# Optimization experiments

Measured on AMD Instinct MI355X. Metric: run time of the kernel, lower is better.

## Reference

```python
import jax, jax.numpy as jnp
import numpy as np
from jax import lax

C, NH, HC, HID, P = 192, 8, 64, 512, 16
B, H, W = 2, 128, 128
EPS = 1e-5


def setup_inputs() -> dict:
    key = jax.random.key(0)
    ks = jax.random.split(key, 12)
    f = lambda i, shape: jax.random.normal(ks[i], shape, jnp.float32) * 0.05
    return dict(
        x=jax.random.normal(ks[0], (B, C, H, W), jnp.float32),
        ln1_g=jnp.ones((C,), jnp.float32), ln1_b=jnp.zeros((C,), jnp.float32),
        wq=f(1, (HID, C)), wk=f(2, (HID, C)), wv=f(3, (HID, C)),
        wo=f(4, (C, HID)), bo=jnp.zeros((C,), jnp.float32),
        dw_w=f(5, (C, 1, 3, 3)), dw_b=jnp.zeros((C,), jnp.float32),
        mlp_w=f(6, (C, 2 * C)), mlp_b=jnp.zeros((C,), jnp.float32),
        ln2_g=jnp.ones((C,), jnp.float32), ln2_b=jnp.zeros((C,), jnp.float32),
        c1_w=f(7, (C, C)), c1_b=jnp.zeros((C,), jnp.float32),
        res_w=f(8, (C, 1, 3, 3)), res_b=jnp.zeros((C,), jnp.float32),
        c2_w=f(9, (C, C)), c2_b=jnp.zeros((C,), jnp.float32),
    )


def ln_ch(x, g, b):
    # LayerNorm over the channel dim of an NCHW tensor (biased variance, like torch)
    m = x.mean(1, keepdims=True)
    v = ((x - m) ** 2).mean(1, keepdims=True)
    return (x - m) / jnp.sqrt(v + EPS) * g[None, :, None, None] + b[None, :, None, None]


def inorm(x):
    # InstanceNorm2d, affine=False
    m = x.mean((2, 3), keepdims=True)
    v = ((x - m) ** 2).mean((2, 3), keepdims=True)
    return (x - m) / jnp.sqrt(v + EPS)


def conv1x1(x, w, b=None):
    y = jnp.einsum('oc,bchw->bohw', w, x)
    return y if b is None else y + b[None, :, None, None]


def dwconv(x, w, b):
    y = lax.conv_general_dilated(x, w, (1, 1), 'SAME',
                                 feature_group_count=x.shape[1],
                                 dimension_numbers=('NCHW', 'OIHW', 'NCHW'))
    return y + b[None, :, None, None]


def res_block(x, w, b):
    return jax.nn.gelu(inorm(dwconv(x, w, b)), approximate=False) + x


def dpsa(x, ln_g, ln_b, wq, wk, wv, wo, bo):
    Bs, _, Hs, Ws = x.shape
    xn = ln_ch(x, ln_g, ln_b)

    def proj(w):  # -> (B*NH, H, W, HC)
        t = jnp.einsum('oc,bchw->bohw', w, xn)
        return t.reshape(Bs * NH, HC, Hs, Ws).transpose(0, 2, 3, 1)

    l2n = lambda t: t / jnp.maximum(jnp.linalg.norm(t, axis=-1, keepdims=True), 1e-12)
    q = l2n(proj(wq))
    k = l2n(proj(wk))
    v = proj(wv)

    qs = q.sum((1, 2))                                   # (BH, HC)
    h_scores = jnp.einsum('bc,bhc->bh', qs, k.sum(2))    # (BH, H)
    w_scores = jnp.einsum('bc,bwc->bw', qs, k.sum(1))    # (BH, W)
    _, h_idx = lax.top_k(h_scores, P)
    _, w_idx = lax.top_k(w_scores, P)

    k = jnp.take_along_axis(k, h_idx[:, :, None, None], axis=1)   # (BH, P, W, HC)
    v = jnp.take_along_axis(v, h_idx[:, :, None, None], axis=1)
    k = jnp.take_along_axis(k, w_idx[:, None, :, None], axis=2)   # (BH, P, P, HC)
    v = jnp.take_along_axis(v, w_idx[:, None, :, None], axis=2)

    qf = q.reshape(Bs * NH, Hs * Ws, HC)
    kf = k.reshape(Bs * NH, P * P, HC)
    vf = v.reshape(Bs * NH, P * P, HC)
    attn = jax.nn.softmax(jnp.einsum('bqc,bkc->bqk', qf, kf), axis=-1)
    out = jnp.einsum('bqk,bkc->bqc', attn, vf)
    out = out.reshape(Bs, NH, Hs, Ws, HC).transpose(0, 1, 4, 2, 3).reshape(Bs, NH * HC, Hs, Ws)
    return conv1x1(out, wo, bo)


def reference(x, ln1_g, ln1_b, wq, wk, wv, wo, bo, dw_w, dw_b, mlp_w, mlp_b,
              ln2_g, ln2_b, c1_w, c1_b, res_w, res_b, c2_w, c2_b):
    global_branch = dpsa(x, ln1_g, ln1_b, wq, wk, wv, wo, bo)
    local_branch = dwconv(x, dw_w, dw_b)
    f = jnp.concatenate((local_branch, global_branch), axis=1)
    f = conv1x1(f, mlp_w, mlp_b) + x
    y = ln_ch(f, ln2_g, ln2_b)
    y = jax.nn.gelu(inorm(conv1x1(y, c1_w, c1_b)), approximate=False)
    y = res_block(y, res_w, res_b)
    y = inorm(conv1x1(y, c2_w, c2_b))
    return y
```

## Files before the change

kernel.cpp:

```cpp
#include <hip/hip_runtime.h>
#include <math.h>

constexpr int kC   = 192;
constexpr int kNH  = 8;
constexpr int kHC  = 64;
constexpr int kHID = 512;
constexpr int kP   = 16;
constexpr int kB   = 2;
constexpr int kH   = 128;
constexpr int kW   = 128;
constexpr int kHW  = kH * kW;
constexpr int kN   = kB * kHW;
constexpr float kEPS = 1e-5f;

typedef __attribute__((ext_vector_type(8))) short bf16x8;
typedef __attribute__((ext_vector_type(4))) float f32x4;

__device__ inline unsigned short f2bf(float f) {
    unsigned int u = __builtin_bit_cast(unsigned int, f);
    unsigned int r = (u + 0x7FFFu + ((u >> 16) & 1u)) >> 16;
    return (unsigned short)r;
}
__device__ inline float bf2f(unsigned short u) {
    return __builtin_bit_cast(float, (unsigned int)u << 16);
}
__device__ inline unsigned int cvtpk(float lo, float hi) {
    unsigned int r;
    asm("v_cvt_pk_bf16_f32 %0, %1, %2" : "=v"(r) : "v"(lo), "v"(hi));
    return r;
}
__device__ inline unsigned long long pk4(float a, float b, float c, float d) {
    return (unsigned long long)cvtpk(a, b) | ((unsigned long long)cvtpk(c, d) << 32);
}
__device__ inline f32x4 ubf4(unsigned long long u) {
    f32x4 r;
    r[0] = bf2f((unsigned short)u);
    r[1] = bf2f((unsigned short)(u >> 16));
    r[2] = bf2f((unsigned short)(u >> 32));
    r[3] = bf2f((unsigned short)(u >> 48));
    return r;
}
__device__ inline float gelu_f(float x) {
    return 0.5f * x * (1.0f + erff(x * 0.70710678118654752f));
}

__global__ void prep_kernel(float* __restrict__ zbase,
                            const float* wq, const float* wk, const float* wm,
                            const float* c1, const float* c2,
                            const float* wo, const float* mlp_b, const float* bo,
                            unsigned short* wqb, unsigned short* wkb,
                            unsigned short* mlpb1, unsigned short* c1b, unsigned short* c2b,
                            unsigned short* w2pb, float* bp2)
{
    int i = blockIdx.x * 256 + threadIdx.x;
    if (i < 2304) { zbase[i] = 0.f; return; }
    i -= 2304;
    if (i < 98304) { wqb[i] = f2bf(wq[i]); return; }
    i -= 98304;
    if (i < 98304) { wkb[i] = f2bf(wk[i]); return; }
    i -= 98304;
    if (i < 36864) { int o = i / 192, k = i - o * 192; mlpb1[i] = f2bf(wm[o * 384 + k]); return; }
    i -= 36864;
    if (i < 36864) { c1b[i] = f2bf(c1[i]); return; }
    i -= 36864;
    if (i < 36864) { c2b[i] = f2bf(c2[i]); return; }
    i -= 36864;
    if (i < 98304) {
        int o = i >> 9, j = i & 511;
        const float* a = wm + o * 384 + 192;
        float s = 0.f;
        for (int c = 0; c < 192; ++c) s += a[c] * wo[c * 512 + j];
        w2pb[o * 512 + j] = f2bf(s);
        if (j == 0) {
            float t = mlp_b[o];
            for (int c = 0; c < 192; ++c) t += a[c] * bo[c];
            bp2[o] = t;
        }
    }
}

__global__ __launch_bounds__(256) void txln_kernel(const float* __restrict__ x,
                                                   unsigned short* __restrict__ xpb,
                                                   unsigned short* __restrict__ xnb,
                                                   const float* __restrict__ g,
                                                   const float* __restrict__ bb)
{
    __shared__ float tile[192][65];
    __shared__ float red[2][4][64];
    __shared__ float pms[64], prs[64];
    int hw0 = blockIdx.x * 64;
    int b   = blockIdx.y;
    int tid = threadIdx.x;
    for (int i = tid; i < 192 * 64; i += 256) {
        int c = i >> 6, p = i & 63;
        tile[c][p] = x[(size_t)(b * kC + c) * kHW + hw0 + p];
    }
    __syncthreads();
    {
        int p = tid & 63, qt = tid >> 6;
        float s = 0.f, ss = 0.f;
        for (int c = qt * 48; c < qt * 48 + 48; ++c) {
            float v = tile[c][p]; s += v; ss += v * v;
        }
        red[0][qt][p] = s; red[1][qt][p] = ss;
    }
    __syncthreads();
    if (tid < 64) {
        float s  = red[0][0][tid] + red[0][1][tid] + red[0][2][tid] + red[0][3][tid];
        float ss = red[1][0][tid] + red[1][1][tid] + red[1][2][tid] + red[1][3][tid];
        float m = s * (1.0f / kC);
        float var = ss * (1.0f / kC) - m * m;
        pms[tid] = m;
        prs[tid] = rsqrtf(var + kEPS);
    }
    __syncthreads();
    for (int i = tid; i < 64 * 192; i += 256) {
        int p = i / 192, c = i - p * 192;
        float raw = tile[c][p];
        size_t oi = (size_t)(b * kHW + hw0 + p) * kC + c;
        xpb[oi] = f2bf(raw);
        xnb[oi] = f2bf((raw - pms[p]) * prs[p] * g[c] + bb[c]);
    }
}

__global__ void ln_pm_bf16_kernel(const unsigned short* __restrict__ in,
                                  unsigned short* __restrict__ out,
                                  const float* __restrict__ g, const float* __restrict__ bb)
{
    int t = blockIdx.x * 256 + threadIdx.x;
    int n = t >> 2, q = t & 3;
    const unsigned long long* ip = (const unsigned long long*)(in + (size_t)n * kC) + q * 12;
    f32x4 v[12];
    float s = 0.f, ss = 0.f;
#pragma unroll
    for (int r = 0; r < 12; ++r) {
        v[r] = ubf4(ip[r]);
        s  += (v[r][0] + v[r][1]) + (v[r][2] + v[r][3]);
        ss += (v[r][0]*v[r][0] + v[r][1]*v[r][1]) + (v[r][2]*v[r][2] + v[r][3]*v[r][3]);
    }
    s  += __shfl_xor(s, 1);  s  += __shfl_xor(s, 2);
    ss += __shfl_xor(ss, 1); ss += __shfl_xor(ss, 2);
    float m  = s * (1.0f / kC);
    float var = ss * (1.0f / kC) - m * m;
    float rs = rsqrtf(var + kEPS);
    unsigned long long* op = (unsigned long long*)(out + (size_t)n * kC) + q * 12;
#pragma unroll
    for (int r = 0; r < 12; ++r) {
        f32x4 gg = *(const f32x4*)(g + q * 48 + r * 4);
        f32x4 bv = *(const f32x4*)(bb + q * 48 + r * 4);
        op[r] = pk4((v[r][0]-m)*rs*gg[0] + bv[0], (v[r][1]-m)*rs*gg[1] + bv[1],
                    (v[r][2]-m)*rs*gg[2] + bv[2], (v[r][3]-m)*rs*gg[3] + bv[3]);
    }
}

#define MGEMM_CORE(KVAL, APTR, BPTR)                                              \
    {                                                                             \
        const unsigned short* Ap = APTR;                                          \
        const unsigned short* Bp = BPTR;                                          \
        _Pragma("unroll 2")                                                       \
        for (int k = 0; k < KVAL; k += 32) {                                      \
            bf16x8 a0 = *(const bf16x8*)(Ap + k);                                 \
            bf16x8 a1 = *(const bf16x8*)(Ap + (size_t)16 * KVAL + k);             \
            bf16x8 b0 = *(const bf16x8*)(Bp + k);                                 \
            bf16x8 b1 = *(const bf16x8*)(Bp + (size_t)16 * KVAL + k);             \
            bf16x8 b2 = *(const bf16x8*)(Bp + (size_t)32 * KVAL + k);             \
            bf16x8 b3 = *(const bf16x8*)(Bp + (size_t)48 * KVAL + k);             \
            acc[0][0] = __builtin_amdgcn_mfma_f32_16x16x32_bf16(a0, b0, acc[0][0], 0, 0, 0); \
            acc[0][1] = __builtin_amdgcn_mfma_f32_16x16x32_bf16(a0, b1, acc[0][1], 0, 0, 0); \
            acc[0][2] = __builtin_amdgcn_mfma_f32_16x16x32_bf16(a0, b2, acc[0][2], 0, 0, 0); \
            acc[0][3] = __builtin_amdgcn_mfma_f32_16x16x32_bf16(a0, b3, acc[0][3], 0, 0, 0); \
            acc[1][0] = __builtin_amdgcn_mfma_f32_16x16x32_bf16(a1, b0, acc[1][0], 0, 0, 0); \
            acc[1][1] = __builtin_amdgcn_mfma_f32_16x16x32_bf16(a1, b1, acc[1][1], 0, 0, 0); \
            acc[1][2] = __builtin_amdgcn_mfma_f32_16x16x32_bf16(a1, b2, acc[1][2], 0, 0, 0); \
            acc[1][3] = __builtin_amdgcn_mfma_f32_16x16x32_bf16(a1, b3, acc[1][3], 0, 0, 0); \
        }                                                                         \
    }

__device__ void mgemm_l2_body(int nblk, int head,
                              const unsigned short* __restrict__ A,
                              const unsigned short* __restrict__ B,
                              unsigned short* __restrict__ out,
                              float* __restrict__ red_out)
{
    __shared__ float ssq[2][2][4][16];
    __shared__ float rbuf[2][2][4][2][4];
    int nB = nblk * 128, oB = head * 64;
    int w = threadIdx.x >> 6, lane = threadIdx.x & 63;
    int l15 = lane & 15, g = lane >> 4;
    int wm = w & 1, wn = w >> 1;

    f32x4 acc[2][4];
#pragma unroll
    for (int mt = 0; mt < 2; ++mt)
#pragma unroll
        for (int nt = 0; nt < 4; ++nt) acc[mt][nt] = (f32x4){0.f,0.f,0.f,0.f};

    MGEMM_CORE(192, A + (size_t)(oB + wm * 32 + l15) * 192 + 8 * g,
                    B + (size_t)(nB + wn * 64 + l15) * 192 + 8 * g);

#pragma unroll
    for (int nt = 0; nt < 4; ++nt) {
        float s = 0.f;
#pragma unroll
        for (int mt = 0; mt < 2; ++mt) {
            f32x4 a = acc[mt][nt];
            s += (a[0]*a[0] + a[1]*a[1]) + (a[2]*a[2] + a[3]*a[3]);
        }
        s += __shfl_xor(s, 16);
        s += __shfl_xor(s, 32);
        if (g == 0) ssq[wm][wn][nt][l15] = s;
    }
    __syncthreads();

    float sc[4];
#pragma unroll
    for (int nt = 0; nt < 4; ++nt) {
        float ss2 = ssq[0][wn][nt][l15] + ssq[1][wn][nt][l15];
        sc[nt] = 1.0f / fmaxf(sqrtf(ss2), 1e-12f);
    }

#pragma unroll
    for (int nt = 0; nt < 4; ++nt) {
        int n = nB + wn * 64 + nt * 16 + l15;
#pragma unroll
        for (int mt = 0; mt < 2; ++mt) {
            int o = oB + wm * 32 + mt * 16 + 4 * g;
            f32x4 v = acc[mt][nt];
            *(unsigned long long*)(out + (size_t)n * kHID + o) =
                pk4(v[0]*sc[nt], v[1]*sc[nt], v[2]*sc[nt], v[3]*sc[nt]);
        }
    }

    float sred[2][4] = {};
#pragma unroll
    for (int nt = 0; nt < 4; ++nt)
#pragma unroll
        for (int mt = 0; mt < 2; ++mt) {
            f32x4 a = acc[mt][nt];
            sred[mt][0] += a[0] * sc[nt];
            sred[mt][1] += a[1] * sc[nt];
            sred[mt][2] += a[2] * sc[nt];
            sred[mt][3] += a[3] * sc[nt];
        }
#pragma unroll
    for (int off = 1; off < 16; off <<= 1)
#pragma unroll
        for (int mt = 0; mt < 2; ++mt)
#pragma unroll
            for (int r = 0; r < 4; ++r)
                sred[mt][r] += __shfl_xor(sred[mt][r], off);
    if (l15 == 0)
#pragma unroll
        for (int mt = 0; mt < 2; ++mt)
#pragma unroll
            for (int r = 0; r < 4; ++r)
                rbuf[wm][wn][g][mt][r] = sred[mt][r];
    __syncthreads();
    if (threadIdx.x < 64) {
        int o = threadIdx.x;
        int wm2 = o >> 5, mt2 = (o >> 4) & 1, g2 = (o >> 2) & 3, r2 = o & 3;
        float v = rbuf[wm2][0][g2][mt2][r2] + rbuf[wm2][1][g2][mt2][r2];
        int row = (nB & (kHW - 1)) >> 7;
        int b = nB >> 14;
        int bh = b * 8 + head;
        red_out[((size_t)(bh * 128 + row)) * 64 + o] = v;
    }
}

__device__ void dwconv_body(int idx, const unsigned short* __restrict__ in,
                            unsigned short* __restrict__ out,
                            const float* __restrict__ wt, const float* __restrict__ bias)
{
    int n = idx / 48;
    int c0 = (idx - n * 48) * 4;
    int hw = n & (kHW - 1);
    int h = hw >> 7, ww = hw & 127;
    f32x4 s = *(const f32x4*)(bias + c0);
#pragma unroll
    for (int dy = -1; dy <= 1; ++dy) {
        int hh = h + dy;
        if (hh < 0 || hh >= kH) continue;
#pragma unroll
        for (int dx = -1; dx <= 1; ++dx) {
            int wx = ww + dx;
            if (wx < 0 || wx >= kW) continue;
            f32x4 v = ubf4(*(const unsigned long long*)(in + (size_t)(n + dy * kW + dx) * kC + c0));
            int t = (dy + 1) * 3 + (dx + 1);
            s[0] += v[0] * wt[(c0 + 0) * 9 + t];
            s[1] += v[1] * wt[(c0 + 1) * 9 + t];
            s[2] += v[2] * wt[(c0 + 2) * 9 + t];
            s[3] += v[3] * wt[(c0 + 3) * 9 + t];
        }
    }
    *(unsigned long long*)(out + (size_t)n * kC + c0) = pk4(s[0], s[1], s[2], s[3]);
}

__global__ __launch_bounds__(256) void branch_kernel(
    const unsigned short* __restrict__ wqb, const unsigned short* __restrict__ wkb,
    const unsigned short* __restrict__ xnb, const unsigned short* __restrict__ xpb,
    unsigned short* __restrict__ qpb, unsigned short* __restrict__ kpb,
    float* __restrict__ qpart, float* __restrict__ ksum_h,
    unsigned short* __restrict__ lb,
    const float* __restrict__ dw_w, const float* __restrict__ dw_b)
{
    int id = blockIdx.x;
    if (id < 2048) {
        mgemm_l2_body(id & 255, id >> 8, wqb, xnb, qpb, qpart);
    } else if (id < 4096) {
        id -= 2048;
        mgemm_l2_body(id & 255, id >> 8, wkb, xnb, kpb, ksum_h);
    } else {
        dwconv_body((id - 4096) * 256 + threadIdx.x, xpb, lb, dw_w, dw_b);
    }
}

__global__ void sum_h_kernel(const unsigned short* __restrict__ buf, float* __restrict__ out)
{
    __shared__ float red[4][64];
    int w = blockIdx.x, bh = blockIdx.y;
    int hc = threadIdx.x & 63, seg = threadIdx.x >> 6;
    int b = bh >> 3, nh = bh & 7;
    const unsigned short* p = buf + (size_t)(b * kHW + seg * 32 * kW + w) * kHID + nh * kHC + hc;
    float s = 0.f;
    for (int h = 0; h < 32; ++h) s += bf2f(p[(size_t)h * kW * kHID]);
    red[seg][hc] = s;
    __syncthreads();
    if (threadIdx.x < 64)
        out[((size_t)bh * kW + w) * kHC + threadIdx.x] =
            red[0][threadIdx.x] + red[1][threadIdx.x] + red[2][threadIdx.x] + red[3][threadIdx.x];
}

__global__ __launch_bounds__(256) void mgemm_is_kernel(
    const unsigned short* __restrict__ A, const unsigned short* __restrict__ B,
    unsigned short* __restrict__ out, const float* __restrict__ bias,
    float* __restrict__ accp)
{
    __shared__ float sa[2][64], qa[2][64];
    int nB = blockIdx.x * 128, oB = blockIdx.y * 64;
    int w = threadIdx.x >> 6, lane = threadIdx.x & 63;
    int l15 = lane & 15, g = lane >> 4;
    int wm = w & 1, wn = w >> 1;

    f32x4 acc[2][4];
#pragma unroll
    for (int mt = 0; mt < 2; ++mt)
#pragma unroll
        for (int nt = 0; nt < 4; ++nt) acc[mt][nt] = (f32x4){0.f,0.f,0.f,0.f};

    MGEMM_CORE(192, A + (size_t)(oB + wm * 32 + l15) * 192 + 8 * g,
                    B + (size_t)(nB + wn * 64 + l15) * 192 + 8 * g);

    f32x4 vv[2][4];
#pragma unroll
    for (int mt = 0; mt < 2; ++mt)
#pragma unroll
        for (int nt = 0; nt < 4; ++nt) {
            int o = oB + wm * 32 + mt * 16 + 4 * g;
            int n = nB + wn * 64 + nt * 16 + l15;
            f32x4 v = acc[mt][nt] + *(const f32x4*)(bias + o);
            vv[mt][nt] = v;
            *(unsigned long long*)(out + (size_t)n * kC + o) = pk4(v[0], v[1], v[2], v[3]);
        }
    float s2[2][4] = {}, q2[2][4] = {};
#pragma unroll
    for (int mt = 0; mt < 2; ++mt)
#pragma unroll
        for (int nt = 0; nt < 4; ++nt)
#pragma unroll
            for (int r = 0; r < 4; ++r) {
                float v = vv[mt][nt][r];
                s2[mt][r] += v; q2[mt][r] += v * v;
            }
#pragma unroll
    for (int off = 1; off < 16; off <<= 1)
#pragma unroll
        for (int mt = 0; mt < 2; ++mt)
#pragma unroll
            for (int r = 0; r < 4; ++r) {
                s2[mt][r] += __shfl_xor(s2[mt][r], off);
                q2[mt][r] += __shfl_xor(q2[mt][r], off);
            }
    if (l15 == 0)
#pragma unroll
        for (int mt = 0; mt < 2; ++mt)
#pragma unroll
            for (int r = 0; r < 4; ++r) {
                int ol = wm * 32 + mt * 16 + 4 * g + r;
                sa[wn][ol] = s2[mt][r];
                qa[wn][ol] = q2[mt][r];
            }
    __syncthreads();
    if (threadIdx.x < 128) {
        int ol = threadIdx.x & 63, st = threadIdx.x >> 6;
        float v = st ? (qa[0][ol] + qa[1][ol]) : (sa[0][ol] + sa[1][ol]);
        int b = nB >> 14;
        atomicAdd(&accp[(size_t)(b * kC + oB + ol) * 2 + st], v);
    }
}

__global__ __launch_bounds__(256) void mgemm_mlp_kernel(
    const unsigned short* __restrict__ A1, const unsigned short* __restrict__ B1,
    const unsigned short* __restrict__ A2, const unsigned short* __restrict__ B2,
    unsigned short* __restrict__ out, const float* __restrict__ bp2,
    const unsigned short* __restrict__ res)
{
    int nB = blockIdx.x * 128, oB = blockIdx.y * 64;
    int w = threadIdx.x >> 6, lane = threadIdx.x & 63;
    int l15 = lane & 15, g = lane >> 4;
    int wm = w & 1, wn = w >> 1;

    f32x4 acc[2][4];
#pragma unroll
    for (int mt = 0; mt < 2; ++mt)
#pragma unroll
        for (int nt = 0; nt < 4; ++nt) acc[mt][nt] = (f32x4){0.f,0.f,0.f,0.f};

    MGEMM_CORE(192, A1 + (size_t)(oB + wm * 32 + l15) * 192 + 8 * g,
                    B1 + (size_t)(nB + wn * 64 + l15) * 192 + 8 * g);
    MGEMM_CORE(512, A2 + (size_t)(oB + wm * 32 + l15) * 512 + 8 * g,
                    B2 + (size_t)(nB + wn * 64 + l15) * 512 + 8 * g);

#pragma unroll
    for (int mt = 0; mt < 2; ++mt)
#pragma unroll
        for (int nt = 0; nt < 4; ++nt) {
            int o = oB + wm * 32 + mt * 16 + 4 * g;
            int n = nB + wn * 64 + nt * 16 + l15;
            f32x4 v = acc[mt][nt];
            v[0] += bp2[o]; v[1] += bp2[o+1]; v[2] += bp2[o+2]; v[3] += bp2[o+3];
            v += ubf4(*(const unsigned long long*)(res + (size_t)n * kC + o));
            *(unsigned long long*)(out + (size_t)n * kC + o) = pk4(v[0], v[1], v[2], v[3]);
        }
}

__global__ void score_topk_kernel(const float* __restrict__ qpart,
                                  const float* __restrict__ ksum_h,
                                  const float* __restrict__ ksum_w,
                                  int* __restrict__ hidx, int* __restrict__ widx)
{
    __shared__ float qsl[2][64];
    __shared__ float hs[128], ws[128];
    int bh = blockIdx.x;
    int tid = threadIdx.x;
    int hc = tid & 63, grp = tid >> 6;
    {
        const float* qp = qpart + ((size_t)bh * 128 + grp * 64) * 64 + hc;
        float s = 0.f;
        for (int i = 0; i < 64; ++i) s += qp[(size_t)i * 64];
        qsl[grp][hc] = s;
    }
    __syncthreads();
    if (tid < 64) qsl[0][tid] += qsl[1][tid];
    __syncthreads();
    {
        const float* kh = ksum_h + ((size_t)bh * 128 + tid) * 64;
        const float* kw = ksum_w + ((size_t)bh * 128 + tid) * 64;
        float sh = 0.f, sw = 0.f;
        for (int c = 0; c < 64; ++c) {
            float q = qsl[0][c];
            sh += q * kh[c];
            sw += q * kw[c];
        }
        hs[tid] = sh; ws[tid] = sw;
    }
    __syncthreads();
    int sel = tid >> 6;
    const float* sc = sel ? ws : hs;
    int* out = (sel ? widx : hidx) + bh * kP;
    int lane = tid & 63;
    float v0 = sc[lane], v1 = sc[lane + 64];
    int i0 = lane, i1 = lane + 64;
    for (int p = 0; p < kP; ++p) {
        float bv; int bi;
        if (v1 > v0) { bv = v1; bi = i1; } else { bv = v0; bi = i0; }
#pragma unroll
        for (int off = 1; off < 64; off <<= 1) {
            float ov = __shfl_xor(bv, off);
            int   oi = __shfl_xor(bi, off);
            if (ov > bv || (ov == bv && oi < bi)) { bv = ov; bi = oi; }
        }
        if (lane == 0) out[p] = bi;
        if (i0 == bi) v0 = -INFINITY;
        if (i1 == bi) v1 = -INFINITY;
    }
}

__global__ void gather_kv_kernel(const unsigned short* __restrict__ kpb,
                                 const unsigned short* __restrict__ xnb,
                                 const float* __restrict__ wv,
                                 const int* __restrict__ hidx, const int* __restrict__ widx,
                                 unsigned short* __restrict__ kf, unsigned short* __restrict__ vfT)
{
    int bh = blockIdx.y, p1 = blockIdx.x;
    int b = bh >> 3, nh = bh & 7;
    int hc = threadIdx.x & 63, pg = threadIdx.x >> 6;
    int hrow = hidx[bh * kP + p1];
    int o = nh * kHC + hc;
    const float* wvp = wv + (size_t)o * kC;
    for (int p2 = pg; p2 < kP; p2 += 4) {
        int wcol = widx[bh * kP + p2];
        int n = b * kHW + hrow * kW + wcol;
        int kidx = p1 * kP + p2;
        kf[((size_t)bh * 256 + kidx) * 64 + hc] = kpb[(size_t)n * kHID + nh * kHC + hc];
        const unsigned int* xr = (const unsigned int*)(xnb + (size_t)n * kC);
        float s = 0.f;
        for (int c2 = 0; c2 < kC / 2; ++c2) {
            unsigned int u = xr[c2];
            s += wvp[c2 * 2]     * bf2f((unsigned short)(u & 0xffff));
            s += wvp[c2 * 2 + 1] * bf2f((unsigned short)(u >> 16));
        }
        vfT[((size_t)bh * 64 + hc) * 256 + kidx] = f2bf(s);
    }
}

__global__ __launch_bounds__(256) void attn_kernel(
    const unsigned short* __restrict__ qpb, unsigned short* __restrict__ ob,
    const unsigned short* __restrict__ kf, const unsigned short* __restrict__ vfT)
{
    __shared__ unsigned short pls[64 * 256];
    __shared__ float lred[4][4][16];

    int bh = blockIdx.y; int b = bh >> 3, nh = bh & 7;
    int nbase = b * kHW + blockIdx.x * 128;
    int tid = threadIdx.x;
    int w = tid >> 6, lane = tid & 63, l15 = lane & 15, g = lane >> 4;

    const unsigned short* kfb = kf + (size_t)bh * 256 * 64;
    bf16x8 ak[4][2];
#pragma unroll
    for (int mt = 0; mt < 4; ++mt)
#pragma unroll
        for (int kt = 0; kt < 2; ++kt)
            ak[mt][kt] = *(const bf16x8*)&kfb[(size_t)(w * 64 + mt * 16 + l15) * 64 + kt * 32 + 8 * g];

    const unsigned short* vfb = vfT + (size_t)bh * 64 * 256;

#pragma unroll
    for (int sub = 0; sub < 2; ++sub) {
        int n0 = nbase + sub * 64;
        bf16x8 bq[4][2];
#pragma unroll
        for (int nt = 0; nt < 4; ++nt)
#pragma unroll
            for (int kt = 0; kt < 2; ++kt)
                bq[nt][kt] = *(const bf16x8*)(qpb + (size_t)(n0 + nt * 16 + l15) * kHID
                                              + nh * kHC + kt * 32 + 8 * g);

        f32x4 acc[4][4];
#pragma unroll
        for (int mt = 0; mt < 4; ++mt)
#pragma unroll
            for (int nt = 0; nt < 4; ++nt) acc[mt][nt] = (f32x4){0.f,0.f,0.f,0.f};

#pragma unroll
        for (int kt = 0; kt < 2; ++kt)
#pragma unroll
            for (int mt = 0; mt < 4; ++mt)
#pragma unroll
                for (int nt = 0; nt < 4; ++nt)
                    acc[mt][nt] = __builtin_amdgcn_mfma_f32_16x16x32_bf16(
                        ak[mt][kt], bq[nt][kt], acc[mt][nt], 0, 0, 0);

        if (sub) __syncthreads();

        float lpart[4] = {0.f, 0.f, 0.f, 0.f};
#pragma unroll
        for (int mt = 0; mt < 4; ++mt)
#pragma unroll
            for (int nt = 0; nt < 4; ++nt) {
                float e0 = __expf(acc[mt][nt][0]);
                float e1 = __expf(acc[mt][nt][1]);
                float e2 = __expf(acc[mt][nt][2]);
                float e3 = __expf(acc[mt][nt][3]);
                lpart[nt] += (e0 + e1) + (e2 + e3);
                int qq = nt * 16 + l15;
                int k0 = w * 64 + mt * 16 + 4 * g;
                int kx = k0 ^ ((qq & 7) << 3);
                *(unsigned long long*)&pls[qq * 256 + kx] = pk4(e0, e1, e2, e3);
            }
#pragma unroll
        for (int nt = 0; nt < 4; ++nt) {
            lpart[nt] += __shfl_xor(lpart[nt], 16);
            lpart[nt] += __shfl_xor(lpart[nt], 32);
        }
        if (g == 0)
#pragma unroll
            for (int nt = 0; nt < 4; ++nt) lred[w][nt][l15] = lpart[nt];
        __syncthreads();

        f32x4 oacc[4];
#pragma unroll
        for (int nt = 0; nt < 4; ++nt) oacc[nt] = (f32x4){0.f,0.f,0.f,0.f};

#pragma unroll
        for (int ks = 0; ks < 8; ++ks) {
            bf16x8 av = *(const bf16x8*)&vfb[(size_t)(w * 16 + l15) * 256 + ks * 32 + 8 * g];
#pragma unroll
            for (int nt = 0; nt < 4; ++nt) {
                int qq = nt * 16 + l15;
                int kx = (ks * 32 + 8 * g) ^ ((qq & 7) << 3);
                bf16x8 bp = *(const bf16x8*)&pls[qq * 256 + kx];
                oacc[nt] = __builtin_amdgcn_mfma_f32_16x16x32_bf16(av, bp, oacc[nt], 0, 0, 0);
            }
        }

#pragma unroll
        for (int nt = 0; nt < 4; ++nt) {
            float l = lred[0][nt][l15] + lred[1][nt][l15] + lred[2][nt][l15] + lred[3][nt][l15];
            float inv = 1.0f / l;
            int qq = nt * 16 + l15;
            int hc0 = w * 16 + 4 * g;
            *(unsigned long long*)(ob + (size_t)(n0 + qq) * kHID + nh * kHC + hc0) =
                pk4(oacc[nt][0] * inv, oacc[nt][1] * inv, oacc[nt][2] * inv, oacc[nt][3] * inv);
        }
    }
}

__global__ void istats_bf16_kernel(const unsigned short* __restrict__ in, float* __restrict__ acc)
{
    int n0 = blockIdx.x * 64;
    int b = n0 >> 14;
    int c = threadIdx.x;
    float s = 0.f, ss = 0.f;
    for (int p = 0; p < 64; ++p) {
        float v = bf2f(in[(size_t)(n0 + p) * kC + c]);
        s += v; ss += v * v;
    }
    atomicAdd(&acc[(size_t)(b * kC + c) * 2],     s);
    atomicAdd(&acc[(size_t)(b * kC + c) * 2 + 1], ss);
}

__device__ inline void inorm_ms(const float* acc, int b, int c, float& m, float& rs)
{
    float s  = acc[(size_t)(b * kC + c) * 2];
    float ss = acc[(size_t)(b * kC + c) * 2 + 1];
    m = s * (1.0f / kHW);
    float var = ss * (1.0f / kHW) - m * m;
    rs = rsqrtf(var + kEPS);
}

__global__ void dwconv_gelu_kernel(const unsigned short* __restrict__ t1,
                                   const float* __restrict__ acc0,
                                   unsigned short* __restrict__ rout,
                                   const float* __restrict__ wt, const float* __restrict__ bias)
{
    int idx = blockIdx.x * 256 + threadIdx.x;
    int n = idx / 48;
    int c0 = (idx - n * 48) * 4;
    int hw = n & (kHW - 1);
    int b = n >> 14;
    int h = hw >> 7, ww = hw & 127;
    float m[4], rs[4];
#pragma unroll
    for (int j = 0; j < 4; ++j) inorm_ms(acc0, b, c0 + j, m[j], rs[j]);
    f32x4 s = *(const f32x4*)(bias + c0);
#pragma unroll
    for (int dy = -1; dy <= 1; ++dy) {
        int hh = h + dy;
        if (hh < 0 || hh >= kH) continue;
#pragma unroll
        for (int dx = -1; dx <= 1; ++dx) {
            int wx = ww + dx;
            if (wx < 0 || wx >= kW) continue;
            f32x4 v = ubf4(*(const unsigned long long*)(t1 + (size_t)(n + dy * kW + dx) * kC + c0));
            int t = (dy + 1) * 3 + (dx + 1);
#pragma unroll
            for (int j = 0; j < 4; ++j)
                s[j] += gelu_f((v[j] - m[j]) * rs[j]) * wt[(c0 + j) * 9 + t];
        }
    }
    *(unsigned long long*)(rout + (size_t)n * kC + c0) = pk4(s[0], s[1], s[2], s[3]);
}

__global__ void apply_res_kernel(const unsigned short* __restrict__ r,
                                 const unsigned short* __restrict__ t1,
                                 const float* __restrict__ acc1, const float* __restrict__ acc0,
                                 unsigned short* __restrict__ out)
{
    int idx = blockIdx.x * 256 + threadIdx.x;
    int n = idx / 48;
    int c0 = (idx - n * 48) * 4;
    int b = n >> 14;
    f32x4 vr = ubf4(*(const unsigned long long*)(r  + (size_t)n * kC + c0));
    f32x4 vt = ubf4(*(const unsigned long long*)(t1 + (size_t)n * kC + c0));
    f32x4 o;
#pragma unroll
    for (int j = 0; j < 4; ++j) {
        float m1, rs1, m0, rs0;
        inorm_ms(acc1, b, c0 + j, m1, rs1);
        inorm_ms(acc0, b, c0 + j, m0, rs0);
        o[j] = gelu_f((vr[j] - m1) * rs1) + gelu_f((vt[j] - m0) * rs0);
    }
    *(unsigned long long*)(out + (size_t)n * kC + c0) = pk4(o[0], o[1], o[2], o[3]);
}

__global__ __launch_bounds__(256) void final_kernel(const unsigned short* __restrict__ in,
                                                    const float* __restrict__ acc,
                                                    float* __restrict__ out)
{
    __shared__ unsigned short tile[192][68];
    int n0 = blockIdx.x * 64;
    int b = n0 >> 14;
    int hw0 = n0 & (kHW - 1);
    int tid = threadIdx.x;
    for (int i = tid; i < 64 * 48; i += 256) {
        int p = i / 48, cq = i - p * 48;
        unsigned long long u = *(const unsigned long long*)(in + (size_t)(n0 + p) * kC + cq * 4);
        tile[cq * 4 + 0][p] = (unsigned short)u;
        tile[cq * 4 + 1][p] = (unsigned short)(u >> 16);
        tile[cq * 4 + 2][p] = (unsigned short)(u >> 32);
        tile[cq * 4 + 3][p] = (unsigned short)(u >> 48);
    }
    __syncthreads();
    for (int i = tid; i < 192 * 16; i += 256) {
        int c = i >> 4, grp = i & 15;
        float m, rs;
        inorm_ms(acc, b, c, m, rs);
        f32x4 o;
#pragma unroll
        for (int j = 0; j < 4; ++j)
            o[j] = (bf2f(tile[c][grp * 4 + j]) - m) * rs;
        *(f32x4*)(out + (size_t)(b * kC + c) * kHW + hw0 + grp * 4) = o;
    }
}

extern "C" void kernel_launch(void* const* d_in, const int* in_sizes, int n_in,
                              void* d_out, int out_size, void* d_ws, size_t ws_size,
                              hipStream_t stream)
{
    const float* x     = (const float*)d_in[0];
    const float* ln1_g = (const float*)d_in[1];
    const float* ln1_b = (const float*)d_in[2];
    const float* wq    = (const float*)d_in[3];
    const float* wk    = (const float*)d_in[4];
    const float* wv    = (const float*)d_in[5];
    const float* wo    = (const float*)d_in[6];
    const float* bo    = (const float*)d_in[7];
    const float* dw_w  = (const float*)d_in[8];
    const float* dw_b  = (const float*)d_in[9];
    const float* mlp_w = (const float*)d_in[10];
    const float* mlp_b = (const float*)d_in[11];
    const float* ln2_g = (const float*)d_in[12];
    const float* ln2_b = (const float*)d_in[13];
    const float* c1_w  = (const float*)d_in[14];
    const float* c1_b  = (const float*)d_in[15];
    const float* res_w = (const float*)d_in[16];
    const float* res_b = (const float*)d_in[17];
    const float* c2_w  = (const float*)d_in[18];
    const float* c2_b  = (const float*)d_in[19];

    char* base = (char*)d_ws;
    unsigned short* XPb = (unsigned short*)(base);
    unsigned short* XNb = (unsigned short*)(base + 25165824);
    unsigned short* QPb = (unsigned short*)(base + 37748736);
    unsigned short* F   = QPb;
    unsigned short* T2  = QPb;
    unsigned short* KPb = (unsigned short*)(base + 71303168);
    unsigned short* OB  = KPb;
    unsigned short* R   = KPb;
    unsigned short* LB  = (unsigned short*)(base + 104857600);
    unsigned short* Y3  = LB;
    unsigned short* T1  = (unsigned short*)(base + 117440512);
    char* sm = base + 130023424;
    float* qpart  = (float*)(sm);                 sm += 524288;
    float* ksum_h = (float*)(sm);                 sm += 524288;
    float* ksum_w = (float*)(sm);                 sm += 524288;
    float* acc0   = (float*)(sm);                 sm += 3072;
    float* acc1   = (float*)(sm);                 sm += 3072;
    float* acc2   = (float*)(sm);                 sm += 3072;
    unsigned short* kf   = (unsigned short*)(sm); sm += 524288;
    unsigned short* vfT  = (unsigned short*)(sm); sm += 524288;
    unsigned short* wqb  = (unsigned short*)(sm); sm += 196608;
    unsigned short* wkb  = (unsigned short*)(sm); sm += 196608;
    unsigned short* mlpb1= (unsigned short*)(sm); sm += 73728;
    unsigned short* c1b  = (unsigned short*)(sm); sm += 73728;
    unsigned short* c2b  = (unsigned short*)(sm); sm += 73728;
    unsigned short* w2pb = (unsigned short*)(sm); sm += 196608;
    float* bp2 = (float*)(sm);                    sm += 1024;
    int* hidx = (int*)(sm);                       sm += 1024;
    int* widx = (int*)(sm);

    prep_kernel<<<1593, 256, 0, stream>>>(acc0, wq, wk, mlp_w, c1_w, c2_w,
                                          wo, mlp_b, bo,
                                          wqb, wkb, mlpb1, c1b, c2b, w2pb, bp2);
    txln_kernel<<<dim3(kHW / 64, kB), 256, 0, stream>>>(x, XPb, XNb, ln1_g, ln1_b);
    branch_kernel<<<10240, 256, 0, stream>>>(wqb, wkb, XNb, XPb, QPb, KPb,
                                             qpart, ksum_h, LB, dw_w, dw_b);
    sum_h_kernel<<<dim3(kW, 16), 256, 0, stream>>>(KPb, ksum_w);
    score_topk_kernel<<<16, 128, 0, stream>>>(qpart, ksum_h, ksum_w, hidx, widx);
    gather_kv_kernel<<<dim3(kP, 16), 256, 0, stream>>>(KPb, XNb, wv, hidx, widx, kf, vfT);
    attn_kernel<<<dim3(kHW / 128, 16), 256, 0, stream>>>(QPb, OB, kf, vfT);
    mgemm_mlp_kernel<<<dim3(kN / 128, kC / 64), 256, 0, stream>>>(mlpb1, LB, w2pb, OB, F, bp2, XPb);
    ln_pm_bf16_kernel<<<(kN * 4) / 256, 256, 0, stream>>>(F, XNb, ln2_g, ln2_b);
    mgemm_is_kernel<<<dim3(kN / 128, kC / 64), 256, 0, stream>>>(c1b, XNb, T1, c1_b, acc0);
    dwconv_gelu_kernel<<<(kN * 48) / 256, 256, 0, stream>>>(T1, acc0, R, res_w, res_b);
    istats_bf16_kernel<<<kN / 64, 192, 0, stream>>>(R, acc1);
    apply_res_kernel<<<(kN * 48) / 256, 256, 0, stream>>>(R, T1, acc1, acc0, Y3);
    mgemm_is_kernel<<<dim3(kN / 128, kC / 64), 256, 0, stream>>>(c2b, Y3, T2, c2_b, acc2);
    final_kernel<<<kN / 64, 256, 0, stream>>>(T2, acc2, (float*)d_out);
}
```

Before: 484.9 us.

## Split Q/K projection into larger-tile GEMM kernel and separate dwconv launch

The combined branch kernel is replaced by a dedicated Q/K projection kernel in which each wave computes a 64x64 tile covering a full head, and the depthwise conv now runs as its own launch. Because each wave owns a whole head's channels, the L2-norm sum of squares is reduced in registers and the shared-memory exchange plus one barrier go away, and each block handles two heads so the activation loads are reused more. The price is higher register pressure (16 accumulators per wave), a smaller grid for the GEMM, and the loss of overlap between the GEMM and the conv inside a single launch.

Measured after the change: 467.0 us. 3.7% less time.

```diff
diff --git a/kernel.cpp b/kernel.cpp
--- a/kernel.cpp
+++ b/kernel.cpp
@@ -176,66 +176,78 @@
         }                                                                         \
     }
 
-__device__ void mgemm_l2_body(int nblk, int head,
-                              const unsigned short* __restrict__ A,
-                              const unsigned short* __restrict__ B,
-                              unsigned short* __restrict__ out,
-                              float* __restrict__ red_out)
-{
-    __shared__ float ssq[2][2][4][16];
-    __shared__ float rbuf[2][2][4][2][4];
-    int nB = nblk * 128, oB = head * 64;
+__global__ __launch_bounds__(256) void qk_proj_kernel(
+    const unsigned short* __restrict__ wqb, const unsigned short* __restrict__ wkb,
+    const unsigned short* __restrict__ xnb,
+    unsigned short* __restrict__ qpb, unsigned short* __restrict__ kpb,
+    float* __restrict__ qpart, float* __restrict__ ksum_h)
+{
+    __shared__ float rbuf[2][2][4][4][4];
+    int nB = blockIdx.x * 128;
+    int hp = blockIdx.y;
+    const unsigned short* A = blockIdx.z ? wkb : wqb;
+    unsigned short* out = blockIdx.z ? kpb : qpb;
+    float* red_out = blockIdx.z ? ksum_h : qpart;
+
     int w = threadIdx.x >> 6, lane = threadIdx.x & 63;
     int l15 = lane & 15, g = lane >> 4;
     int wm = w & 1, wn = w >> 1;
-
-    f32x4 acc[2][4];
-#pragma unroll
-    for (int mt = 0; mt < 2; ++mt)
+    int oB = hp * 128;
+
+    const unsigned short* Ap = A + (size_t)(oB + wm * 64 + l15) * 192 + 8 * g;
+    const unsigned short* Bp = xnb + (size_t)(nB + wn * 64 + l15) * 192 + 8 * g;
+
+    f32x4 acc[4][4];
+#pragma unroll
+    for (int mt = 0; mt < 4; ++mt)
 #pragma unroll
         for (int nt = 0; nt < 4; ++nt) acc[mt][nt] = (f32x4){0.f,0.f,0.f,0.f};
 
-    MGEMM_CORE(192, A + (size_t)(oB + wm * 32 + l15) * 192 + 8 * g,
-                    B + (size_t)(nB + wn * 64 + l15) * 192 + 8 * g);
-
+#pragma unroll 2
+    for (int k = 0; k < 192; k += 32) {
+        bf16x8 a[4], bb[4];
+#pragma unroll
+        for (int mt = 0; mt < 4; ++mt) a[mt] = *(const bf16x8*)(Ap + (size_t)mt * 16 * 192 + k);
+#pragma unroll
+        for (int nt = 0; nt < 4; ++nt) bb[nt] = *(const bf16x8*)(Bp + (size_t)nt * 16 * 192 + k);
+#pragma unroll
+        for (int mt = 0; mt < 4; ++mt)
+#pragma unroll
+            for (int nt = 0; nt < 4; ++nt)
+                acc[mt][nt] = __builtin_amdgcn_mfma_f32_16x16x32_bf16(a[mt], bb[nt], acc[mt][nt], 0, 0, 0);
+    }
+
+    float sc[4];
 #pragma unroll
     for (int nt = 0; nt < 4; ++nt) {
         float s = 0.f;
 #pragma unroll
-        for (int mt = 0; mt < 2; ++mt) {
+        for (int mt = 0; mt < 4; ++mt) {
             f32x4 a = acc[mt][nt];
             s += (a[0]*a[0] + a[1]*a[1]) + (a[2]*a[2] + a[3]*a[3]);
         }
         s += __shfl_xor(s, 16);
         s += __shfl_xor(s, 32);
-        if (g == 0) ssq[wm][wn][nt][l15] = s;
-    }
-    __syncthreads();
-
-    float sc[4];
-#pragma unroll
-    for (int nt = 0; nt < 4; ++nt) {
-        float ss2 = ssq[0][wn][nt][l15] + ssq[1][wn][nt][l15];
-        sc[nt] = 1.0f / fmaxf(sqrtf(ss2), 1e-12f);
+        sc[nt] = 1.0f / fmaxf(sqrtf(s), 1e-12f);
     }
 
 #pragma unroll
     for (int nt = 0; nt < 4; ++nt) {
         int n = nB + wn * 64 + nt * 16 + l15;
 #pragma unroll
-        for (int mt = 0; mt < 2; ++mt) {
-            int o = oB + wm * 32 + mt * 16 + 4 * g;
+        for (int mt = 0; mt < 4; ++mt) {
+            int o = oB + wm * 64 + mt * 16 + 4 * g;
             f32x4 v = acc[mt][nt];
             *(unsigned long long*)(out + (size_t)n * kHID + o) =
                 pk4(v[0]*sc[nt], v[1]*sc[nt], v[2]*sc[nt], v[3]*sc[nt]);
         }
     }
 
-    float sred[2][4] = {};
+    float sred[4][4] = {};
 #pragma unroll
     for (int nt = 0; nt < 4; ++nt)
 #pragma unroll
-        for (int mt = 0; mt < 2; ++mt) {
+        for (int mt = 0; mt < 4; ++mt) {
             f32x4 a = acc[mt][nt];
             sred[mt][0] += a[0] * sc[nt];
             sred[mt][1] += a[1] * sc[nt];
@@ -245,32 +257,34 @@
 #pragma unroll
     for (int off = 1; off < 16; off <<= 1)
 #pragma unroll
-        for (int mt = 0; mt < 2; ++mt)
+        for (int mt = 0; mt < 4; ++mt)
 #pragma unroll
             for (int r = 0; r < 4; ++r)
                 sred[mt][r] += __shfl_xor(sred[mt][r], off);
     if (l15 == 0)
 #pragma unroll
-        for (int mt = 0; mt < 2; ++mt)
+        for (int mt = 0; mt < 4; ++mt)
 #pragma unroll
             for (int r = 0; r < 4; ++r)
                 rbuf[wm][wn][g][mt][r] = sred[mt][r];
     __syncthreads();
-    if (threadIdx.x < 64) {
-        int o = threadIdx.x;
-        int wm2 = o >> 5, mt2 = (o >> 4) & 1, g2 = (o >> 2) & 3, r2 = o & 3;
+    if (threadIdx.x < 128) {
+        int wm2 = threadIdx.x >> 6;
+        int o = threadIdx.x & 63;
+        int mt2 = o >> 4, g2 = (o >> 2) & 3, r2 = o & 3;
         float v = rbuf[wm2][0][g2][mt2][r2] + rbuf[wm2][1][g2][mt2][r2];
         int row = (nB & (kHW - 1)) >> 7;
         int b = nB >> 14;
-        int bh = b * 8 + head;
+        int bh = b * 8 + hp * 2 + wm2;
         red_out[((size_t)(bh * 128 + row)) * 64 + o] = v;
     }
 }
 
-__device__ void dwconv_body(int idx, const unsigned short* __restrict__ in,
-                            unsigned short* __restrict__ out,
-                            const float* __restrict__ wt, const float* __restrict__ bias)
-{
+__global__ void dwconv_pm_kernel(const unsigned short* __restrict__ in,
+                                 unsigned short* __restrict__ out,
+                                 const float* __restrict__ wt, const float* __restrict__ bias)
+{
+    int idx = blockIdx.x * 256 + threadIdx.x;
     int n = idx / 48;
     int c0 = (idx - n * 48) * 4;
     int hw = n & (kHW - 1);
@@ -293,25 +307,6 @@
         }
     }
     *(unsigned long long*)(out + (size_t)n * kC + c0) = pk4(s[0], s[1], s[2], s[3]);
-}
-
-__global__ __launch_bounds__(256) void branch_kernel(
-    const unsigned short* __restrict__ wqb, const unsigned short* __restrict__ wkb,
-    const unsigned short* __restrict__ xnb, const unsigned short* __restrict__ xpb,
-    unsigned short* __restrict__ qpb, unsigned short* __restrict__ kpb,
-    float* __restrict__ qpart, float* __restrict__ ksum_h,
-    unsigned short* __restrict__ lb,
-    const float* __restrict__ dw_w, const float* __restrict__ dw_b)
-{
-    int id = blockIdx.x;
-    if (id < 2048) {
-        mgemm_l2_body(id & 255, id >> 8, wqb, xnb, qpb, qpart);
-    } else if (id < 4096) {
-        id -= 2048;
-        mgemm_l2_body(id & 255, id >> 8, wkb, xnb, kpb, ksum_h);
-    } else {
-        dwconv_body((id - 4096) * 256 + threadIdx.x, xpb, lb, dw_w, dw_b);
-    }
 }
 
 __global__ void sum_h_kernel(const unsigned short* __restrict__ buf, float* __restrict__ out)
@@ -784,8 +779,9 @@
                                           wo, mlp_b, bo,
                                           wqb, wkb, mlpb1, c1b, c2b, w2pb, bp2);
     txln_kernel<<<dim3(kHW / 64, kB), 256, 0, stream>>>(x, XPb, XNb, ln1_g, ln1_b);
-    branch_kernel<<<10240, 256, 0, stream>>>(wqb, wkb, XNb, XPb, QPb, KPb,
-                                             qpart, ksum_h, LB, dw_w, dw_b);
+    qk_proj_kernel<<<dim3(kN / 128, 4, 2), 256, 0, stream>>>(wqb, wkb, XNb, QPb, KPb,
+                                                             qpart, ksum_h);
+    dwconv_pm_kernel<<<(kN * 48) / 256, 256, 0, stream>>>(XPb, LB, dw_w, dw_b);
     sum_h_kernel<<<dim3(kW, 16), 256, 0, stream>>>(KPb, ksum_w);
     score_topk_kernel<<<16, 128, 0, stream>>>(qpart, ksum_h, ksum_w, hidx, widx);
     gather_kv_kernel<<<dim3(kP, 16), 256, 0, stream>>>(KPb, XNb, wv, hidx, widx, kf, vfT);
```
